# Optimization experiments

Measured on AMD Instinct MI355X. Metric: run time of the kernel, lower is better.

The kernel has to match this reference:

```python
import jax, jax.numpy as jnp
import numpy as np

D = 256  # feature_dim
NQ = 512
NK = 512


def setup_inputs() -> dict:
    key = jax.random.key(0)
    ks = jax.random.split(key, 12)
    s = 0.05
    return {
        "x": jax.random.normal(ks[0], (1, D, NQ), dtype=jnp.float32),
        "source": jax.random.normal(ks[1], (1, D, NK), dtype=jnp.float32),
        "dist": jax.random.normal(ks[2], (1, D, NQ * NK), dtype=jnp.float32),
        "mask": jax.random.randint(ks[3], (NQ, NK), 0, 2).astype(jnp.bool_),
        # MLPAttention mlp: channels [3D, D, 1] (1x1 convs == per-position matmuls)
        "aW1": jax.random.normal(ks[4], (D, 3 * D), dtype=jnp.float32) * s,
        "ab1": jax.random.normal(ks[5], (D,), dtype=jnp.float32) * s,
        "aW2": jax.random.normal(ks[6], (1, D), dtype=jnp.float32) * s,
        "ab2": jax.random.normal(ks[7], (1,), dtype=jnp.float32) * s,
        # merge mlp: channels [2D, 2D, D], last bias initialized to 0
        "mW1": jax.random.normal(ks[8], (2 * D, 2 * D), dtype=jnp.float32) * s,
        "mb1": jax.random.normal(ks[9], (2 * D,), dtype=jnp.float32) * s,
        "mW2": jax.random.normal(ks[10], (D, 2 * D), dtype=jnp.float32) * s,
        "mb2": jnp.zeros((D,), dtype=jnp.float32),
    }


def _conv1x1(W, b, x):
    # Conv1d(kernel_size=1): (out,in) @ (b,in,n) -> (b,out,n)
    return jnp.einsum('oc,bcn->bon', W, x) + b[None, :, None]


def reference(x, source, dist, mask, aW1, ab1, aW2, ab2, mW1, mb1, mW2, mb2):
    nq, nk = x.shape[-1], source.shape[-1]
    d = x.shape[1]
    # broadcast query over keys and key over queries, flatten to (1, d, nq*nk)
    qb = jnp.broadcast_to(x[:, :, :, None], (1, d, nq, nk)).reshape(1, d, nq * nk)
    kb = jnp.broadcast_to(source[:, :, None, :], (1, d, nq, nk)).reshape(1, d, nq * nk)
    feat = jnp.concatenate([qb, kb, dist], axis=1)  # (1, 3d, nq*nk)
    h = jax.nn.relu(_conv1x1(aW1, ab1, feat))       # (1, d, nq*nk)
    scores = _conv1x1(aW2, ab2, h).reshape(1, nq, nk)
    # boolean-mask branch: push masked-out entries far below the min
    neg = jax.lax.stop_gradient(scores.min()) - 20.0
    scores = scores + neg * (~mask).astype(scores.dtype)[None]
    prob = jax.nn.softmax(scores, axis=-1)
    message = jnp.einsum('bnm,bdm->bdn', prob, source)  # value == source
    # merge MLP on concat([x, message])
    cat = jnp.concatenate([x, message], axis=1)  # (1, 2d, nq)
    h2 = jax.nn.relu(_conv1x1(mW1, mb1, cat))
    out = _conv1x1(mW2, mb2, h2)  # (1, d, nq)
    return (out, scores)
```

## Files before the change

kernel.cpp:

```cpp
#include <hip/hip_runtime.h>
#include <stdint.h>

#define D_ 256
#define NQ_ 512
#define NK_ 512
#define NP_ (NQ_*NK_)

typedef __attribute__((ext_vector_type(8))) __bf16 bf16x8;
typedef __attribute__((ext_vector_type(4))) float f32x4;

__device__ __forceinline__ unsigned short f2bf(float f) {
  unsigned u = __builtin_bit_cast(unsigned, f);
  u += 0x7FFFu + ((u >> 16) & 1u);
  return (unsigned short)(u >> 16);
}
__device__ __forceinline__ unsigned encf(float f) {
  unsigned u = __builtin_bit_cast(unsigned, f);
  return (u & 0x80000000u) ? ~u : (u | 0x80000000u);
}
__device__ __forceinline__ float decf(unsigned e) {
  unsigned u = (e & 0x80000000u) ? (e ^ 0x80000000u) : ~e;
  return __builtin_bit_cast(float, u);
}

__global__ void kinit(const unsigned* __restrict__ maskw,
                      unsigned* __restrict__ wsMin, unsigned* __restrict__ wsFlag) {
  int l = threadIdx.x;
  unsigned a01 = 1, af = 1;
  for (int i = 0; i < 4; ++i) {
    unsigned v = maskw[l*4 + i];
    a01 &= (v == 0u || v == 1u) ? 1u : 0u;
    af  &= (v == 0u || v == 0x3f800000u) ? 1u : 0u;
  }
  unsigned long long b01 = __ballot(a01 != 0), bf = __ballot(af != 0);
  if (l == 0) {
    *wsFlag = (b01 == ~0ull) ? 1u : ((bf == ~0ull) ? 2u : 0u);
    *wsMin = 0xFFFFFFFFu;
  }
}

__global__ __launch_bounds__(256) void kconvert(
    const float* __restrict__ aW1, const float* __restrict__ source,
    const float* __restrict__ x, const float* __restrict__ mW1,
    const float* __restrict__ mW2,
    unsigned short* __restrict__ Cb, unsigned short* __restrict__ srcbf,
    unsigned short* __restrict__ srcT, unsigned short* __restrict__ mW1b,
    unsigned short* __restrict__ mW2b, unsigned short* __restrict__ aW1A,
    unsigned short* __restrict__ aW1B, unsigned short* __restrict__ catT) {
  const int b = blockIdx.x, t = threadIdx.x;
  if (b < 704) {
    const float* src; unsigned short* dst;
    if (b < 64)        { int j = b*1024 + t*4;       int e=j>>8, c=j&255; src = aW1 + e*768 + 512 + c; dst = Cb + j; }
    else if (b < 192)  { int j = (b-64)*1024 + t*4;  src = source + j;    dst = srcbf + j; }
    else if (b < 448)  { int j = (b-192)*1024 + t*4; src = mW1 + j;       dst = mW1b + j; }
    else if (b < 576)  { int j = (b-448)*1024 + t*4; src = mW2 + j;       dst = mW2b + j; }
    else if (b < 640)  { int j = (b-576)*1024 + t*4; int e=j>>8, c=j&255; src = aW1 + e*768 + c;       dst = aW1A + j; }
    else               { int j = (b-640)*1024 + t*4; int e=j>>8, c=j&255; src = aW1 + e*768 + 256 + c; dst = aW1B + j; }
    const float4 v = *(const float4*)src;
    ushort4 o; o.x=f2bf(v.x); o.y=f2bf(v.y); o.z=f2bf(v.z); o.w=f2bf(v.w);
    *(ushort4*)dst = o;
  } else if (b < 1216) {
    int qq = b - 704;
    catT[qq*512 + t] = f2bf(x[(size_t)t*512 + qq]);
  } else {
    int kk = b - 1216;
    srcT[kk*256 + t] = f2bf(source[(size_t)t*512 + kk]);
  }
}

template<int EPI, int KTILES>
__global__ __launch_bounds__(256) void gemm_k(
    const unsigned short* __restrict__ A, int lda,
    const unsigned short* __restrict__ B, int ldb,
    const float* __restrict__ bias,
    void* __restrict__ Dst, int ldd, int nTilesN) {
  const int t = threadIdx.x, w = t >> 6, l = t & 63, l15 = l & 15, g = l >> 4;
  const int bm = blockIdx.x / nTilesN, bn = blockIdx.x % nTilesN;
  const int m0 = bm*64 + w*16, n0 = bn*64;
  const unsigned short* Ap = A + (size_t)(m0 + l15)*lda + g*8;
  const unsigned short* Bp = B + (size_t)(n0 + l15)*ldb + g*8;
  f32x4 acc[4];
  #pragma unroll
  for (int n = 0; n < 4; ++n) acc[n] = (f32x4){0.f,0.f,0.f,0.f};
  #pragma unroll 2
  for (int kk = 0; kk < KTILES; ++kk) {
    bf16x8 a = *(const bf16x8*)(Ap + kk*32);
    #pragma unroll
    for (int n = 0; n < 4; ++n) {
      bf16x8 b = *(const bf16x8*)(Bp + (size_t)n*16*ldb + kk*32);
      acc[n] = __builtin_amdgcn_mfma_f32_16x16x32_bf16(a, b, acc[n], 0, 0, 0);
    }
  }
  #pragma unroll
  for (int n = 0; n < 4; ++n) {
    const int col = n0 + n*16 + l15;
    const float bc = (EPI & 4) ? bias[col] : 0.f;
    #pragma unroll
    for (int r = 0; r < 4; ++r) {
      const int m = m0 + g*4 + r;
      float v = acc[n][r] + bc;
      if (EPI & 8) v += bias[m];
      if (EPI & 2) v = fmaxf(v, 0.f);
      if (EPI & 1) ((unsigned short*)Dst)[(size_t)m*ldd + col] = f2bf(v);
      else         ((float*)Dst)[(size_t)m*ldd + col] = v;
    }
  }
}

__global__ __launch_bounds__(256) void kscores(
    const float* __restrict__ dist, const unsigned short* __restrict__ Cb,
    const float* __restrict__ Up, const float* __restrict__ Vm,
    const float* __restrict__ aW2, const float* __restrict__ ab2,
    float* __restrict__ outScores, unsigned* __restrict__ wsMin) {
  __shared__ __align__(16) unsigned char ldsB[2][64*64];
  __shared__ float u_s[256], aw2_s[256];
  __shared__ float red[4][64];

  const int t = threadIdx.x;
  const int w = t >> 6;
  const int l = t & 63;
  const int l15 = l & 15;
  const int g = l >> 4;

  const int p0 = blockIdx.x * 64;
  const int q  = p0 >> 9;
  const int k0 = p0 & 511;

  u_s[t]   = Up[q*256 + t];
  aw2_s[t] = aW2[t];

  f32x4 acc[4][4];
  #pragma unroll
  for (int m = 0; m < 4; ++m)
    #pragma unroll
    for (int n = 0; n < 4; ++n) acc[m][n] = (f32x4){0.f, 0.f, 0.f, 0.f};

  const int keyoff = ((g ^ ((l15 >> 1) & 3)) << 4);
  const int quad1 = (w + g) & 3;
  const int quad2 = quad1 + 4;
  const int wr1 = l*64 + (((quad1 >> 1) ^ ((l >> 1) & 3)) << 4) + ((quad1 & 1) << 3);
  const int wr2 = l*64 + (((quad2 >> 1) ^ ((l >> 1) & 3)) << 4) + ((quad2 & 1) << 3);

  float v0[4], v1[4];
  #pragma unroll
  for (int i = 0; i < 4; ++i) v0[i] = dist[(size_t)(quad1*4 + i)*NP_ + p0 + l];
  #pragma unroll
  for (int i = 0; i < 4; ++i) v1[i] = dist[(size_t)(quad2*4 + i)*NP_ + p0 + l];

  int buf = 0;
  for (int kk = 0; kk < 8; ++kk) {
    *(uint2*)(&ldsB[buf][wr1]) = make_uint2(
        (unsigned)f2bf(v0[0]) | ((unsigned)f2bf(v0[1]) << 16),
        (unsigned)f2bf(v0[2]) | ((unsigned)f2bf(v0[3]) << 16));
    *(uint2*)(&ldsB[buf][wr2]) = make_uint2(
        (unsigned)f2bf(v1[0]) | ((unsigned)f2bf(v1[1]) << 16),
        (unsigned)f2bf(v1[2]) | ((unsigned)f2bf(v1[3]) << 16));
    if (kk < 7) {
      size_t base = (size_t)((kk + 1) * 32) * NP_ + (size_t)(p0 + l);
      #pragma unroll
      for (int i = 0; i < 4; ++i) v0[i] = dist[base + (size_t)(quad1*4 + i) * NP_];
      #pragma unroll
      for (int i = 0; i < 4; ++i) v1[i] = dist[base + (size_t)(quad2*4 + i) * NP_];
    }
    __syncthreads();
    bf16x8 a[4], b[4];
    #pragma unroll
    for (int m = 0; m < 4; ++m)
      a[m] = *(const bf16x8*)(Cb + (size_t)(w*64 + m*16 + l15)*256 + kk*32 + g*8);
    #pragma unroll
    for (int n = 0; n < 4; ++n)
      b[n] = *(const bf16x8*)(&ldsB[buf][(n*16 + l15)*64 + keyoff]);
    #pragma unroll
    for (int m = 0; m < 4; ++m)
      #pragma unroll
      for (int n = 0; n < 4; ++n)
        acc[m][n] = __builtin_amdgcn_mfma_f32_16x16x32_bf16(a[m], b[n], acc[m][n], 0, 0, 0);
    buf ^= 1;
  }
  __syncthreads();

  float part[4];
  #pragma unroll
  for (int n = 0; n < 4; ++n) {
    int j = k0 + n*16 + l15;
    float s = 0.f;
    #pragma unroll
    for (int m = 0; m < 4; ++m) {
      #pragma unroll
      for (int r = 0; r < 4; ++r) {
        int e = w*64 + m*16 + g*4 + r;
        float gv = acc[m][n][r] + u_s[e] + Vm[e*512 + j];
        s += aw2_s[e] * fmaxf(gv, 0.f);
      }
    }
    s += __shfl_xor(s, 16);
    s += __shfl_xor(s, 32);
    part[n] = s;
  }
  if (l < 16) {
    #pragma unroll
    for (int n = 0; n < 4; ++n) red[w][n*16 + l] = part[n];
  }
  __syncthreads();
  if (t < 64) {
    float s = red[0][t] + red[1][t] + red[2][t] + red[3][t] + ab2[0];
    outScores[p0 + t] = s;
    float mn = s;
    #pragma unroll
    for (int off = 32; off; off >>= 1) mn = fminf(mn, __shfl_xor(mn, off));
    if (t == 0) atomicMin(wsMin, encf(mn));
  }
}

__global__ __launch_bounds__(256) void ksoftmax(
    const void* __restrict__ maskp,
    const unsigned* __restrict__ wsMin, const unsigned* __restrict__ wsFlag,
    float* __restrict__ scores, unsigned short* __restrict__ prob) {
  __shared__ float srow[512];
  __shared__ float redl[8];
  const int t = threadIdx.x, w = t >> 6, l = t & 63;
  const int q = blockIdx.x;
  const float neg = decf(*wsMin) - 20.0f;
  const unsigned flag = *wsFlag;

  for (int k = t; k < 512; k += 256) {
    float raw = scores[q*512 + k];
    bool mv;
    if (flag == 1)      mv = ((const int*)maskp)[q*512 + k] != 0;
    else if (flag == 2) mv = ((const float*)maskp)[q*512 + k] != 0.f;
    else                mv = ((const unsigned char*)maskp)[q*512 + k] != 0;
    float ms = raw + (mv ? 0.f : neg);
    scores[q*512 + k] = ms;
    srow[k] = ms;
  }
  __syncthreads();
  float lm = fmaxf(srow[t], srow[t + 256]);
  #pragma unroll
  for (int off = 32; off; off >>= 1) lm = fmaxf(lm, __shfl_xor(lm, off));
  if (l == 0) redl[w] = lm;
  __syncthreads();
  float rmax = fmaxf(fmaxf(redl[0], redl[1]), fmaxf(redl[2], redl[3]));
  float e0 = __expf(srow[t] - rmax), e1 = __expf(srow[t + 256] - rmax);
  float ls = e0 + e1;
  #pragma unroll
  for (int off = 32; off; off >>= 1) ls += __shfl_xor(ls, off);
  if (l == 0) redl[4 + w] = ls;
  __syncthreads();
  float inv = 1.0f / (redl[4] + redl[5] + redl[6] + redl[7]);
  prob[q*512 + t]       = f2bf(e0 * inv);
  prob[q*512 + t + 256] = f2bf(e1 * inv);
}

extern "C" void kernel_launch(void* const* d_in, const int* in_sizes, int n_in,
                              void* d_out, int out_size, void* d_ws, size_t ws_size,
                              hipStream_t stream) {
  const float* x      = (const float*)d_in[0];
  const float* source = (const float*)d_in[1];
  const float* dist   = (const float*)d_in[2];
  const void*  mask   = (const void*)d_in[3];
  const float* aW1    = (const float*)d_in[4];
  const float* ab1    = (const float*)d_in[5];
  const float* aW2    = (const float*)d_in[6];
  const float* ab2    = (const float*)d_in[7];
  const float* mW1    = (const float*)d_in[8];
  const float* mb1    = (const float*)d_in[9];
  const float* mW2    = (const float*)d_in[10];
  const float* mb2    = (const float*)d_in[11];

  float* outMain = (float*)d_out;
  float* scores  = outMain + 256*512;

  char* ws = (char*)d_ws;
  unsigned* wsMin  = (unsigned*)ws;
  unsigned* wsFlag = wsMin + 1;
  unsigned short* Cb    = (unsigned short*)(ws + 1024);
  float*          Up    = (float*)(ws + 132096);
  float*          Vm    = (float*)(ws + 656384);
  unsigned short* srcbf = (unsigned short*)(ws + 1180672);
  unsigned short* srcT  = (unsigned short*)(ws + 1442816);
  unsigned short* mW1b  = (unsigned short*)(ws + 1704960);
  unsigned short* mW2b  = (unsigned short*)(ws + 2229248);
  unsigned short* aW1A  = (unsigned short*)(ws + 2491392);
  unsigned short* aW1B  = (unsigned short*)(ws + 2622464);
  unsigned short* catT  = (unsigned short*)(ws + 2753536);
  unsigned short* prob  = (unsigned short*)(ws + 3277824);
  unsigned short* h2T   = (unsigned short*)(ws + 3802112);

  hipLaunchKernelGGL(kinit, dim3(1), dim3(64), 0, stream,
                     (const unsigned*)mask, wsMin, wsFlag);
  hipLaunchKernelGGL(kconvert, dim3(1728), dim3(256), 0, stream,
                     aW1, source, x, mW1, mW2, Cb, srcbf, srcT, mW1b, mW2b, aW1A, aW1B, catT);
  hipLaunchKernelGGL((gemm_k<4, 8>),  dim3(32), dim3(256), 0, stream,
                     catT, 512, aW1A, 256, ab1, (void*)Up, 256, 4);
  hipLaunchKernelGGL((gemm_k<0, 8>),  dim3(32), dim3(256), 0, stream,
                     aW1B, 256, srcT, 256, (const float*)nullptr, (void*)Vm, 512, 8);
  hipLaunchKernelGGL(kscores, dim3(4096), dim3(256), 0, stream,
                     dist, Cb, Up, Vm, aW2, ab2, scores, wsMin);
  hipLaunchKernelGGL(ksoftmax, dim3(512), dim3(256), 0, stream,
                     mask, wsMin, wsFlag, scores, prob);
  hipLaunchKernelGGL((gemm_k<1, 16>), dim3(32), dim3(256), 0, stream,
                     prob, 512, srcbf, 512, (const float*)nullptr, (void*)(catT + 256), 512, 4);
  hipLaunchKernelGGL((gemm_k<7, 16>), dim3(64), dim3(256), 0, stream,
                     catT, 512, mW1b, 512, mb1, (void*)h2T, 512, 8);
  hipLaunchKernelGGL((gemm_k<8, 16>), dim3(32), dim3(256), 0, stream,
                     mW2b, 512, h2T, 512, mb2, (void*)outMain, 512, 8);
}
```

Before: 206.1 us.

## Load dist directly into MFMA registers and use tiled LDS transposes

The scores kernel stops staging dist through a double-buffered LDS tile with barriers. Each lane now loads its dist column values straight from global memory, converts them to bf16 in registers and feeds them to the MFMAs. This removes LDS traffic and a sync per k-step, but global loads become 16-lane runs of 64 bytes each, which may lower coalescing efficiency. Separately, the strided single-element transposes of x and source move out of kconvert into a 64x64 LDS-tiled transpose kernel with coalesced float4 reads, at the cost of two extra launches.

```diff
diff --git a/kernel.cpp b/kernel.cpp
--- a/kernel.cpp
+++ b/kernel.cpp
@@ -41,30 +41,44 @@
 
 __global__ __launch_bounds__(256) void kconvert(
     const float* __restrict__ aW1, const float* __restrict__ source,
-    const float* __restrict__ x, const float* __restrict__ mW1,
-    const float* __restrict__ mW2,
+    const float* __restrict__ mW1, const float* __restrict__ mW2,
     unsigned short* __restrict__ Cb, unsigned short* __restrict__ srcbf,
-    unsigned short* __restrict__ srcT, unsigned short* __restrict__ mW1b,
-    unsigned short* __restrict__ mW2b, unsigned short* __restrict__ aW1A,
-    unsigned short* __restrict__ aW1B, unsigned short* __restrict__ catT) {
+    unsigned short* __restrict__ mW1b, unsigned short* __restrict__ mW2b,
+    unsigned short* __restrict__ aW1A, unsigned short* __restrict__ aW1B) {
   const int b = blockIdx.x, t = threadIdx.x;
-  if (b < 704) {
-    const float* src; unsigned short* dst;
-    if (b < 64)        { int j = b*1024 + t*4;       int e=j>>8, c=j&255; src = aW1 + e*768 + 512 + c; dst = Cb + j; }
-    else if (b < 192)  { int j = (b-64)*1024 + t*4;  src = source + j;    dst = srcbf + j; }
-    else if (b < 448)  { int j = (b-192)*1024 + t*4; src = mW1 + j;       dst = mW1b + j; }
-    else if (b < 576)  { int j = (b-448)*1024 + t*4; src = mW2 + j;       dst = mW2b + j; }
-    else if (b < 640)  { int j = (b-576)*1024 + t*4; int e=j>>8, c=j&255; src = aW1 + e*768 + c;       dst = aW1A + j; }
-    else               { int j = (b-640)*1024 + t*4; int e=j>>8, c=j&255; src = aW1 + e*768 + 256 + c; dst = aW1B + j; }
-    const float4 v = *(const float4*)src;
-    ushort4 o; o.x=f2bf(v.x); o.y=f2bf(v.y); o.z=f2bf(v.z); o.w=f2bf(v.w);
-    *(ushort4*)dst = o;
-  } else if (b < 1216) {
-    int qq = b - 704;
-    catT[qq*512 + t] = f2bf(x[(size_t)t*512 + qq]);
-  } else {
-    int kk = b - 1216;
-    srcT[kk*256 + t] = f2bf(source[(size_t)t*512 + kk]);
+  const float* src; unsigned short* dst;
+  if (b < 64)        { int j = b*1024 + t*4;       int e=j>>8, c=j&255; src = aW1 + e*768 + 512 + c; dst = Cb + j; }
+  else if (b < 192)  { int j = (b-64)*1024 + t*4;  src = source + j;    dst = srcbf + j; }
+  else if (b < 448)  { int j = (b-192)*1024 + t*4; src = mW1 + j;       dst = mW1b + j; }
+  else if (b < 576)  { int j = (b-448)*1024 + t*4; src = mW2 + j;       dst = mW2b + j; }
+  else if (b < 640)  { int j = (b-576)*1024 + t*4; int e=j>>8, c=j&255; src = aW1 + e*768 + c;       dst = aW1A + j; }
+  else               { int j = (b-640)*1024 + t*4; int e=j>>8, c=j&255; src = aW1 + e*768 + 256 + c; dst = aW1B + j; }
+  const float4 v = *(const float4*)src;
+  ushort4 o; o.x=f2bf(v.x); o.y=f2bf(v.y); o.z=f2bf(v.z); o.w=f2bf(v.w);
+  *(ushort4*)dst = o;
+}
+
+__global__ __launch_bounds__(256) void ktransp(const float* __restrict__ src,
+                                               unsigned short* __restrict__ dst, int ldd) {
+  __shared__ float tile[64][65];
+  const int bd = blockIdx.x >> 3;
+  const int bq = blockIdx.x & 7;
+  const int t = threadIdx.x;
+  const int r = t >> 4, c4 = (t & 15) * 4;
+  #pragma unroll
+  for (int rr = 0; rr < 4; ++rr) {
+    int dl = rr*16 + r;
+    float4 v = *(const float4*)(src + (size_t)(bd*64 + dl)*512 + bq*64 + c4);
+    tile[dl][c4+0] = v.x; tile[dl][c4+1] = v.y; tile[dl][c4+2] = v.z; tile[dl][c4+3] = v.w;
+  }
+  __syncthreads();
+  #pragma unroll
+  for (int rr = 0; rr < 4; ++rr) {
+    int j = rr*16 + r;
+    ushort4 o;
+    o.x = f2bf(tile[c4+0][j]); o.y = f2bf(tile[c4+1][j]);
+    o.z = f2bf(tile[c4+2][j]); o.w = f2bf(tile[c4+3][j]);
+    *(ushort4*)(dst + (size_t)(bq*64 + j)*ldd + bd*64 + c4) = o;
   }
 }
 
@@ -112,7 +126,6 @@
     const float* __restrict__ Up, const float* __restrict__ Vm,
     const float* __restrict__ aW2, const float* __restrict__ ab2,
     float* __restrict__ outScores, unsigned* __restrict__ wsMin) {
-  __shared__ __align__(16) unsigned char ldsB[2][64*64];
   __shared__ float u_s[256], aw2_s[256];
   __shared__ float red[4][64];
 
@@ -135,47 +148,28 @@
     #pragma unroll
     for (int n = 0; n < 4; ++n) acc[m][n] = (f32x4){0.f, 0.f, 0.f, 0.f};
 
-  const int keyoff = ((g ^ ((l15 >> 1) & 3)) << 4);
-  const int quad1 = (w + g) & 3;
-  const int quad2 = quad1 + 4;
-  const int wr1 = l*64 + (((quad1 >> 1) ^ ((l >> 1) & 3)) << 4) + ((quad1 & 1) << 3);
-  const int wr2 = l*64 + (((quad2 >> 1) ^ ((l >> 1) & 3)) << 4) + ((quad2 & 1) << 3);
-
-  float v0[4], v1[4];
-  #pragma unroll
-  for (int i = 0; i < 4; ++i) v0[i] = dist[(size_t)(quad1*4 + i)*NP_ + p0 + l];
-  #pragma unroll
-  for (int i = 0; i < 4; ++i) v1[i] = dist[(size_t)(quad2*4 + i)*NP_ + p0 + l];
-
-  int buf = 0;
+  const float* drow = dist + (size_t)(g*8)*NP_ + (size_t)(p0 + l15);
+  const unsigned short* Abase = Cb + (size_t)(w*64 + l15)*256 + g*8;
+
+  #pragma unroll 2
   for (int kk = 0; kk < 8; ++kk) {
-    *(uint2*)(&ldsB[buf][wr1]) = make_uint2(
-        (unsigned)f2bf(v0[0]) | ((unsigned)f2bf(v0[1]) << 16),
-        (unsigned)f2bf(v0[2]) | ((unsigned)f2bf(v0[3]) << 16));
-    *(uint2*)(&ldsB[buf][wr2]) = make_uint2(
-        (unsigned)f2bf(v1[0]) | ((unsigned)f2bf(v1[1]) << 16),
-        (unsigned)f2bf(v1[2]) | ((unsigned)f2bf(v1[3]) << 16));
-    if (kk < 7) {
-      size_t base = (size_t)((kk + 1) * 32) * NP_ + (size_t)(p0 + l);
+    bf16x8 a[4];
+    #pragma unroll
+    for (int m = 0; m < 4; ++m)
+      a[m] = *(const bf16x8*)(Abase + (size_t)m*16*256 + kk*32);
+    #pragma unroll
+    for (int n = 0; n < 4; ++n) {
+      float v[8];
       #pragma unroll
-      for (int i = 0; i < 4; ++i) v0[i] = dist[base + (size_t)(quad1*4 + i) * NP_];
+      for (int i = 0; i < 8; ++i)
+        v[i] = drow[(size_t)(kk*32 + i)*NP_ + n*16];
+      bf16x8 b;
       #pragma unroll
-      for (int i = 0; i < 4; ++i) v1[i] = dist[base + (size_t)(quad2*4 + i) * NP_];
+      for (int i = 0; i < 8; ++i) b[i] = (__bf16)v[i];
+      #pragma unroll
+      for (int m = 0; m < 4; ++m)
+        acc[m][n] = __builtin_amdgcn_mfma_f32_16x16x32_bf16(a[m], b, acc[m][n], 0, 0, 0);
     }
-    __syncthreads();
-    bf16x8 a[4], b[4];
-    #pragma unroll
-    for (int m = 0; m < 4; ++m)
-      a[m] = *(const bf16x8*)(Cb + (size_t)(w*64 + m*16 + l15)*256 + kk*32 + g*8);
-    #pragma unroll
-    for (int n = 0; n < 4; ++n)
-      b[n] = *(const bf16x8*)(&ldsB[buf][(n*16 + l15)*64 + keyoff]);
-    #pragma unroll
-    for (int m = 0; m < 4; ++m)
-      #pragma unroll
-      for (int n = 0; n < 4; ++n)
-        acc[m][n] = __builtin_amdgcn_mfma_f32_16x16x32_bf16(a[m], b[n], acc[m][n], 0, 0, 0);
-    buf ^= 1;
   }
   __syncthreads();
 
@@ -288,8 +282,10 @@
 
   hipLaunchKernelGGL(kinit, dim3(1), dim3(64), 0, stream,
                      (const unsigned*)mask, wsMin, wsFlag);
-  hipLaunchKernelGGL(kconvert, dim3(1728), dim3(256), 0, stream,
-                     aW1, source, x, mW1, mW2, Cb, srcbf, srcT, mW1b, mW2b, aW1A, aW1B, catT);
+  hipLaunchKernelGGL(kconvert, dim3(704), dim3(256), 0, stream,
+                     aW1, source, mW1, mW2, Cb, srcbf, mW1b, mW2b, aW1A, aW1B);
+  hipLaunchKernelGGL(ktransp, dim3(32), dim3(256), 0, stream, x, catT, 512);
+  hipLaunchKernelGGL(ktransp, dim3(32), dim3(256), 0, stream, source, srcT, 256);
   hipLaunchKernelGGL((gemm_k<4, 8>),  dim3(32), dim3(256), 0, stream,
                      catT, 512, aW1A, 256, ab1, (void*)Up, 256, 4);
   hipLaunchKernelGGL((gemm_k<0, 8>),  dim3(32), dim3(256), 0, stream,
```

Result: slower. 233.7 us (+13.4%).
